# Kernel tuning notes

Measured on AMD Instinct MI355X. Metric: run time of the kernel, lower is better.

The kernel has to match this reference:

```python
import jax, jax.numpy as jnp
import numpy as np

N_FFT = 1024
HOP = 256
WIN = 1024


def _hann(win_length):
    # torch.hann_window (periodic): 0.5*(1 - cos(2*pi*n/N))
    n = jnp.arange(win_length, dtype=jnp.float32)
    return 0.5 - 0.5 * jnp.cos(2.0 * jnp.pi * n / win_length)


def setup_inputs() -> dict:
    key = jax.random.key(0)
    k1, k2 = jax.random.split(key)
    B, N, T = 16, N_FFT // 2 + 1, 2048
    spec_re = jax.random.normal(k1, (B, N, T), dtype=jnp.float32)
    spec_im = jax.random.normal(k2, (B, N, T), dtype=jnp.float32)
    mask = jnp.ones((B, T), dtype=jnp.float32)
    return {"spec_re": spec_re, "spec_im": spec_im, "mask": mask}


def reference(spec_re, spec_im, mask):
    B, N, T = spec_re.shape
    pad = (WIN - HOP) // 2
    window = _hann(WIN)

    spec = jax.lax.complex(spec_re, spec_im)
    # irfft over frequency axis, norm='backward' is jnp default -> [B, N_FFT, T]
    ifft = jnp.fft.irfft(spec, n=N_FFT, axis=1)
    # fuse window multiply + mask multiply
    frames = ifft * window[None, :, None] * mask[:, None, :]

    L = (T - 1) * HOP + WIN  # fold output size
    idx = jnp.arange(T)[None, :] * HOP + jnp.arange(WIN)[:, None]

    # fold(ifft): overlap-add of frames -> [B, L], then trim padding
    y = jnp.zeros((B, L), frames.dtype).at[:, idx].add(frames)[:, pad:L - pad]

    # window envelope (batch-independent): fold of window^2
    env = jnp.zeros((L,), frames.dtype).at[idx].add(
        jnp.broadcast_to((window * window)[:, None], (WIN, T))
    )[pad:L - pad]
    y = y / env

    # fold of ones*mask -> effective sample mask
    folded_mask = jnp.zeros((B, L), frames.dtype).at[:, idx].add(
        jnp.broadcast_to(mask[:, None, :], (B, WIN, T))
    )[:, pad:L - pad]
    effective_mask = (folded_mask > 0).astype(jnp.float32)
    return (y, effective_mask)
```

## Files before the change

### kernel.cpp

```cpp
#include <hip/hip_runtime.h>

#define THREADS 1024

#define BAR() do { asm volatile("s_waitcnt lgkmcnt(0)" ::: "memory"); \
                   __builtin_amdgcn_s_barrier();                      \
                   asm volatile("" ::: "memory"); } while (0)

__device__ __forceinline__ void dft8(float* vr, float* vi) {
    float t0r=vr[0]+vr[4], t0i=vi[0]+vi[4];
    float t1r=vr[0]-vr[4], t1i=vi[0]-vi[4];
    float t2r=vr[2]+vr[6], t2i=vi[2]+vi[6];
    float t3r=vr[2]-vr[6], t3i=vi[2]-vi[6];
    float t4r=vr[1]+vr[5], t4i=vi[1]+vi[5];
    float t5r=vr[1]-vr[5], t5i=vi[1]-vi[5];
    float t6r=vr[3]+vr[7], t6i=vi[3]+vi[7];
    float t7r=vr[3]-vr[7], t7i=vi[3]-vi[7];
    float e0r=t0r+t2r, e0i=t0i+t2i;
    float e1r=t1r-t3i, e1i=t1i+t3r;
    float e2r=t0r-t2r, e2i=t0i-t2i;
    float e3r=t1r+t3i, e3i=t1i-t3r;
    float o0r=t4r+t6r, o0i=t4i+t6i;
    float o1r=t5r-t7i, o1i=t5i+t7r;
    float o2r=t4r-t6r, o2i=t4i-t6i;
    float o3r=t5r+t7i, o3i=t5i-t7r;
    const float C = 0.70710678118654752f;
    float w1r = C*(o1r - o1i), w1i = C*(o1r + o1i);
    float w2r = -o2i,          w2i = o2r;
    float w3r = -C*(o3r + o3i), w3i = C*(o3r - o3i);
    vr[0]=e0r+o0r; vi[0]=e0i+o0i;
    vr[1]=e1r+w1r; vi[1]=e1i+w1i;
    vr[2]=e2r+w2r; vi[2]=e2i+w2i;
    vr[3]=e3r+w3r; vi[3]=e3i+w3i;
    vr[4]=e0r-o0r; vi[4]=e0i-o0i;
    vr[5]=e1r-w1r; vi[5]=e1i-w1i;
    vr[6]=e2r-w2r; vi[6]=e2i-w2i;
    vr[7]=e3r-w3r; vi[7]=e3i-w3i;
}

__device__ __forceinline__ void fft512(float* Re, float* Im, int l,
                                       const float2* s_twzb, const float2* s_tw64,
                                       const float2* s_tw512) {
    const int a_ = l >> 3, b_ = l & 7;
    float zr[8], zi[8];
    float cw = s_twzb[l].x, sw_ = s_twzb[l].y;
    const float C8 = 0.92387953251128675f, S8 = 0.38268343236508977f;
    #pragma unroll
    for (int k0 = 0; k0 < 8; ++k0) {
        int k = (k0<<6) + l;
        float xkr = Re[k],     xki = Im[k];
        float xmr = Re[512-k], xmi = Im[512-k];
        if (k == 0) { xki = 0.f; xmi = 0.f; }
        float Er = 0.5f*(xkr + xmr), Ei = 0.5f*(xki - xmi);
        float Dr = 0.5f*(xkr - xmr), Di = 0.5f*(xki + xmi);
        float Or = cw*Dr - sw_*Di,  Oi = sw_*Dr + cw*Di;
        zr[k0] = Er - Oi;
        zi[k0] = Ei + Or;
        float nc = cw*C8 - sw_*S8; sw_ = sw_*C8 + cw*S8; cw = nc;
    }
    dft8(zr, zi);
    #pragma unroll
    for (int q = 0; q < 8; ++q) {
        int idx = (q<<6) + l;
        Re[idx ^ (((idx>>6)&7)<<3)] = zr[q];
        Im[idx ^ (((idx>>6)&7)<<3)] = zi[q];
    }
    #pragma unroll
    for (int q = 0; q < 8; ++q) {
        int idx = (a_<<6) + (q<<3) + b_;
        int ph = idx ^ (((idx>>6)&7)<<3);
        zr[q] = Re[ph]; zi[q] = Im[ph];
    }
    {
        float c1 = s_tw64[a_].x, s1 = s_tw64[a_].y;
        float cr = c1, ci = s1;
        #pragma unroll
        for (int q = 1; q < 8; ++q) {
            float tr = zr[q]*cr - zi[q]*ci;
            zi[q] = zr[q]*ci + zi[q]*cr;
            zr[q] = tr;
            float nc = cr*c1 - ci*s1; ci = ci*c1 + cr*s1; cr = nc;
        }
    }
    dft8(zr, zi);
    #pragma unroll
    for (int q = 0; q < 8; ++q) {
        int idx = (b_<<6) + (q<<3) + a_;
        int ph = idx ^ (((idx>>6)&7)<<3);
        Re[ph] = zr[q]; Im[ph] = zi[q];
    }
    #pragma unroll
    for (int q = 0; q < 8; ++q) {
        int idx = (q<<6) + l;
        int ph = idx ^ (((idx>>6)&7)<<3);
        zr[q] = Re[ph]; zi[q] = Im[ph];
    }
    {
        float c1 = s_tw512[l].x, s1 = s_tw512[l].y;
        float cr = c1, ci = s1;
        #pragma unroll
        for (int q = 1; q < 8; ++q) {
            float tr = zr[q]*cr - zi[q]*ci;
            zi[q] = zr[q]*ci + zi[q]*cr;
            zr[q] = tr;
            float nc = cr*c1 - ci*s1; ci = ci*c1 + cr*s1; cr = nc;
        }
    }
    dft8(zr, zi);
    #pragma unroll
    for (int q = 0; q < 8; ++q) {
        Re[(q<<6) + l] = zr[q];
        Im[(q<<6) + l] = zi[q];
    }
}

template<bool USE_WS>
__global__ __launch_bounds__(1024, 8) void istft_main(const float* __restrict__ spec_re,
                                                      const float* __restrict__ spec_im,
                                                      const float* __restrict__ mask,
                                                      float* __restrict__ out,
                                                      float* __restrict__ wsL,
                                                      float* __restrict__ wsR)
{
    const int G   = blockIdx.x;
    const int b   = blockIdx.y;
    const int tid = threadIdx.x;

    __shared__ __attribute__((aligned(16))) float s_slot[16704];
    __shared__ __attribute__((aligned(16))) float s_wt[1024];
    __shared__ __attribute__((aligned(16))) float s_envr[256];
    __shared__ float  s_maskx[22];
    __shared__ float  s_ps[23];
    __shared__ float2 s_twzb[64];
    __shared__ float2 s_tw64[8];
    __shared__ float2 s_tw512[64];

    const size_t base = (size_t)b * 513 * 2048 + (size_t)(G * 16);
    const int c  = tid & 3;
    const int r0 = tid >> 2;
    float4 vr0, vi0, vr1, vi1, nyr, nyi;
    float4 mk;
    float mxv = 0.f;
    {
        size_t o0 = base + (size_t)(r0      ) * 2048 + (size_t)(c * 4);
        size_t o1 = base + (size_t)(r0 + 256) * 2048 + (size_t)(c * 4);
        vr0 = *(const float4*)(spec_re + o0);  vi0 = *(const float4*)(spec_im + o0);
        vr1 = *(const float4*)(spec_re + o1);  vi1 = *(const float4*)(spec_im + o1);
        if (tid < 4) {
            size_t o2 = base + (size_t)512 * 2048 + (size_t)(tid * 4);
            nyr = *(const float4*)(spec_re + o2);
            nyi = *(const float4*)(spec_im + o2);
        }
        mk = *(const float4*)(mask + b*2048 + G*16 + c*4);
        if (tid < 22) {
            int gf = G*16 - 3 + tid;
            mxv = (gf >= 0 && gf < 2048) ? mask[b*2048 + gf] : 0.f;
        }
    }

    {
        float w = 0.5f - 0.5f * __cosf(6.2831853071795864f * (float)tid * (1.0f/1024.0f));
        s_wt[tid] = w * (1.0f/512.0f);
    }
    if (tid < 256) {
        float e = 0.f;
        #pragma unroll
        for (int k = 0; k < 4; ++k) {
            float w = 0.5f - 0.5f * __cosf(6.2831853071795864f * (float)(tid + (k<<8)) * (1.0f/1024.0f));
            e += w * w;
        }
        s_envr[tid] = 1.0f / e;
    }
    if (tid < 64) {
        float s1, c1, s2, c2;
        __sincosf(3.1415926535897932f * (float)tid * (1.0f/512.0f), &s1, &c1);
        s_twzb[tid] = make_float2(c1, s1);
        __sincosf(6.2831853071795864f * (float)tid * (1.0f/512.0f), &s2, &c2);
        s_tw512[tid] = make_float2(c2, s2);
    }
    if (tid < 8) {
        float s3, c3;
        __sincosf(6.2831853071795864f * (float)tid * (1.0f/64.0f), &s3, &c3);
        s_tw64[tid] = make_float2(c3, s3);
    }
    if (tid < 22) s_maskx[tid] = mxv;

    {
        const float* mp = (const float*)&mk;
        #pragma unroll
        for (int f = 0; f < 4; ++f) {
            int fr = (c*4 + f) * 522;
            s_slot[       fr + r0      ] = ((const float*)&vr0)[f] * mp[f];
            s_slot[8352 + fr + r0      ] = ((const float*)&vi0)[f] * mp[f];
            s_slot[       fr + r0 + 256] = ((const float*)&vr1)[f] * mp[f];
            s_slot[8352 + fr + r0 + 256] = ((const float*)&vi1)[f] * mp[f];
        }
        if (tid < 4) {
            #pragma unroll
            for (int f = 0; f < 4; ++f) {
                int fr = (tid*4 + f) * 522;
                s_slot[       fr + 512] = ((const float*)&nyr)[f] * mp[f];
                s_slot[8352 + fr + 512] = ((const float*)&nyi)[f] * mp[f];
            }
        }
    }
    if (tid == 0) {
        float acc = 0.f;
        s_ps[0] = 0.f;
        #pragma unroll
        for (int i = 0; i < 22; ++i) { acc += s_maskx[i]; s_ps[i+1] = acc; }
    }
    BAR();

    __builtin_amdgcn_s_setprio(1);
    {
        const int wv = tid >> 6, l = tid & 63;
        fft512(&s_slot[wv*522], &s_slot[8352 + wv*522], l, s_twzb, s_tw64, s_tw512);
    }
    __builtin_amdgcn_s_setprio(0);
    BAR();

    const int P0 = G << 12;
    float* yout = out + (size_t)b * 524288;
    float* mout = out + 16ull*524288 + (size_t)b * 524288;

    {
        const int p0 = tid << 2;
        if (p0 >= 768) {
            const int F0 = (p0 >> 8) - 3;
            float4 acc = {0.f, 0.f, 0.f, 0.f};
            #pragma unroll
            for (int u = 0; u < 4; ++u) {
                int F = F0 + u;
                int j = p0 - (F << 8);
                float2 re = *(const float2*)&s_slot[       F*522 + (j >> 1)];
                float2 im = *(const float2*)&s_slot[8352 + F*522 + (j >> 1)];
                float4 w4 = *(const float4*)&s_wt[j];
                acc.x += re.x * w4.x;  acc.y += im.x * w4.y;
                acc.z += re.y * w4.z;  acc.w += im.y * w4.w;
            }
            float fm = s_ps[(p0 >> 8) + 4] - s_ps[F0 + 3];
            float m = (fm > 0.f) ? 1.0f : 0.0f;
            float4 er = *(const float4*)&s_envr[p0 & 255];
            int s = P0 + p0 - 384;
            float4 r;
            r.x = acc.x * er.x;  r.y = acc.y * er.y;
            r.z = acc.z * er.z;  r.w = acc.w * er.w;
            *(float4*)&yout[s] = r;
            float4 mm = {m, m, m, m};
            *(float4*)&mout[s] = mm;
        } else {
            const int thi = p0 >> 8;
            float4 acc = {0.f, 0.f, 0.f, 0.f};
            for (int F = 0; F <= thi; ++F) {
                int j = p0 - (F << 8);
                float2 re = *(const float2*)&s_slot[       F*522 + (j >> 1)];
                float2 im = *(const float2*)&s_slot[8352 + F*522 + (j >> 1)];
                float4 w4 = *(const float4*)&s_wt[j];
                acc.x += re.x * w4.x;  acc.y += im.x * w4.y;
                acc.z += re.y * w4.z;  acc.w += im.y * w4.w;
            }
            float fm = s_ps[thi + 4] - s_ps[((p0 - 768) >> 8) + 3];
            float m = (fm > 0.f) ? 1.0f : 0.0f;
            float4 mm = {m, m, m, m};
            if (G == 0) {
                if (p0 >= 384) {
                    float4 e = {0.f, 0.f, 0.f, 0.f};
                    for (int t = 0; t <= thi; ++t) {
                        float4 w4 = *(const float4*)&s_wt[p0 - (t << 8)];
                        e.x += w4.x * w4.x;  e.y += w4.y * w4.y;
                        e.z += w4.z * w4.z;  e.w += w4.w * w4.w;
                    }
                    const float S = 1.0f / 262144.0f;
                    float4 r;
                    r.x = acc.x * S / e.x;  r.y = acc.y * S / e.y;
                    r.z = acc.z * S / e.z;  r.w = acc.w * S / e.w;
                    *(float4*)&yout[p0 - 384] = r;
                    *(float4*)&mout[p0 - 384] = mm;
                }
            } else {
                int s = P0 + p0 - 384;
                if (USE_WS) {
                    *(float4*)&wsL[(size_t)((b << 7) + G) * 768 + p0] = acc;
                } else {
                    atomicAdd(&yout[s+0], acc.x);  atomicAdd(&yout[s+1], acc.y);
                    atomicAdd(&yout[s+2], acc.z);  atomicAdd(&yout[s+3], acc.w);
                }
                *(float4*)&mout[s] = mm;
            }
        }
    }
    if (tid < 192) {
        const int p0 = 4096 + (tid << 2);
        const int Flo = (p0 - 768) >> 8;
        float4 acc = {0.f, 0.f, 0.f, 0.f};
        for (int F = Flo; F < 16; ++F) {
            int j = p0 - (F << 8);
            float2 re = *(const float2*)&s_slot[       F*522 + (j >> 1)];
            float2 im = *(const float2*)&s_slot[8352 + F*522 + (j >> 1)];
            float4 w4 = *(const float4*)&s_wt[j];
            acc.x += re.x * w4.x;  acc.y += im.x * w4.y;
            acc.z += re.y * w4.z;  acc.w += im.y * w4.w;
        }
        float fm = s_ps[min(p0 >> 8, 18) + 4] - s_ps[Flo + 3];
        float m = (fm > 0.f) ? 1.0f : 0.0f;
        float4 mm = {m, m, m, m};
        if (G == 127) {
            if (p0 < 4480) {
                float4 e = {0.f, 0.f, 0.f, 0.f};
                for (int t = Flo; t < 16; ++t) {
                    float4 w4 = *(const float4*)&s_wt[p0 - (t << 8)];
                    e.x += w4.x * w4.x;  e.y += w4.y * w4.y;
                    e.z += w4.z * w4.z;  e.w += w4.w * w4.w;
                }
                const float S = 1.0f / 262144.0f;
                int s = P0 + p0 - 384;
                float4 r;
                r.x = acc.x * S / e.x;  r.y = acc.y * S / e.y;
                r.z = acc.z * S / e.z;  r.w = acc.w * S / e.w;
                *(float4*)&yout[s] = r;
                *(float4*)&mout[s] = mm;
            }
        } else {
            int s = P0 + p0 - 384;
            if (USE_WS) {
                *(float4*)&wsR[(size_t)((b << 7) + G) * 768 + (p0 - 4096)] = acc;
            } else {
                atomicAdd(&yout[s+0], acc.x);  atomicAdd(&yout[s+1], acc.y);
                atomicAdd(&yout[s+2], acc.z);  atomicAdd(&yout[s+3], acc.w);
            }
            *(float4*)&mout[s] = mm;
        }
    }
}

__global__ void istft_fixup_ws(const float* __restrict__ wsL, const float* __restrict__ wsR,
                               float* __restrict__ out) {
    int idx = blockIdx.x * 256 + threadIdx.x;
    if (idx >= 16*127*192) return;
    int q4 = (idx % 192) << 2;
    int t_ = idx / 192;
    int g  = (t_ % 127) + 1;
    int b  = t_ / 127;
    float4 aR = *(const float4*)&wsR[(size_t)((b << 7) + (g-1)) * 768 + q4];
    float4 aL = *(const float4*)&wsL[(size_t)((b << 7) + g) * 768 + q4];
    float4 r;
    #pragma unroll
    for (int cmp = 0; cmp < 4; ++cmp) {
        int j0 = (q4 + cmp) & 255;
        float e = 0.f;
        #pragma unroll
        for (int u = 0; u < 4; ++u) {
            float w = 0.5f - 0.5f * __cosf(6.2831853071795864f * (float)(j0 + (u<<8)) * (1.0f/1024.0f));
            e += w * w;
        }
        float a = ((const float*)&aR)[cmp] + ((const float*)&aL)[cmp];
        ((float*)&r)[cmp] = a / e;
    }
    *(float4*)&out[(size_t)b*524288 + (size_t)((g << 12) + q4 - 384)] = r;
}

__global__ void istft_zero(float* __restrict__ out) {
    int idx = blockIdx.x * 256 + threadIdx.x;
    if (idx >= 16*127*768) return;
    int q  = idx % 768;
    int t_ = idx / 768;
    int g  = (t_ % 127) + 1;
    int b  = t_ / 127;
    out[(size_t)b*524288 + (g << 12) + q - 384] = 0.f;
}

__global__ void istft_fixup_at(float* __restrict__ out) {
    int idx = blockIdx.x * 256 + threadIdx.x;
    if (idx >= 16*127*768) return;
    int q  = idx % 768;
    int t_ = idx / 768;
    int g  = (t_ % 127) + 1;
    int b  = t_ / 127;
    int j0 = q & 255;
    float e = 0.f;
    #pragma unroll
    for (int u = 0; u < 4; ++u) {
        float w = 0.5f - 0.5f * __cosf(6.2831853071795864f * (float)(j0 + (u<<8)) * (1.0f/1024.0f));
        e += w * w;
    }
    size_t o = (size_t)b*524288 + (size_t)((g << 12) + q - 384);
    out[o] = out[o] / e;
}

extern "C" void kernel_launch(void* const* d_in, const int* in_sizes, int n_in,
                              void* d_out, int out_size, void* d_ws, size_t ws_size,
                              hipStream_t stream) {
    (void)in_sizes; (void)n_in; (void)out_size;
    const float* spec_re = (const float*)d_in[0];
    const float* spec_im = (const float*)d_in[1];
    const float* mask    = (const float*)d_in[2];
    float* out = (float*)d_out;
    const size_t ws_need = 2ull * 16 * 128 * 768 * 4;
    if (ws_size >= ws_need && d_ws != nullptr) {
        float* wsL = (float*)d_ws;
        float* wsR = wsL + 16ull*128*768;
        istft_main<true><<<dim3(128, 16), 1024, 0, stream>>>(spec_re, spec_im, mask, out, wsL, wsR);
        const int nq = 16*127*192;
        istft_fixup_ws<<<(nq + 255)/256, 256, 0, stream>>>(wsL, wsR, out);
    } else {
        const int nstrip = 16*127*768;
        istft_zero<<<(nstrip + 255)/256, 256, 0, stream>>>(out);
        istft_main<false><<<dim3(128, 16), 1024, 0, stream>>>(spec_re, spec_im, mask, out, nullptr, nullptr);
        istft_fixup_at<<<(nstrip + 255)/256, 256, 0, stream>>>(out);
    }
}
```

Before: 77.81 us.

## Interleave complex FFT slots as float2 and use full twiddle tables

```diff
diff --git a/kernel.cpp b/kernel.cpp
--- a/kernel.cpp
+++ b/kernel.cpp
@@ -1,10 +1,13 @@
 #include <hip/hip_runtime.h>
 
 #define THREADS 1024
+#define CSTRIDE 514
 
 #define BAR() do { asm volatile("s_waitcnt lgkmcnt(0)" ::: "memory"); \
                    __builtin_amdgcn_s_barrier();                      \
                    asm volatile("" ::: "memory"); } while (0)
+
+__device__ __forceinline__ int swz(int i) { return i ^ (((i >> 6) & 7) << 3); }
 
 __device__ __forceinline__ void dft8(float* vr, float* vi) {
     float t0r=vr[0]+vr[4], t0i=vi[0]+vi[4];
@@ -37,21 +40,21 @@
     vr[7]=e3r-w3r; vi[7]=e3i-w3i;
 }
 
-__device__ __forceinline__ void fft512(float* Re, float* Im, int l,
-                                       const float2* s_twzb, const float2* s_tw64,
-                                       const float2* s_tw512) {
+__device__ __forceinline__ void fft512i(float2* S, int l,
+                                        const float2* twzb, const float2* tw64f,
+                                        const float2* tw512f) {
     const int a_ = l >> 3, b_ = l & 7;
     float zr[8], zi[8];
-    float cw = s_twzb[l].x, sw_ = s_twzb[l].y;
+    float cw = twzb[l].x, sw_ = twzb[l].y;
     const float C8 = 0.92387953251128675f, S8 = 0.38268343236508977f;
     #pragma unroll
     for (int k0 = 0; k0 < 8; ++k0) {
         int k = (k0<<6) + l;
-        float xkr = Re[k],     xki = Im[k];
-        float xmr = Re[512-k], xmi = Im[512-k];
-        if (k == 0) { xki = 0.f; xmi = 0.f; }
-        float Er = 0.5f*(xkr + xmr), Ei = 0.5f*(xki - xmi);
-        float Dr = 0.5f*(xkr - xmr), Di = 0.5f*(xki + xmi);
+        float2 xk = S[swz(k)];
+        float2 xm = S[swz(512-k)];
+        if (k == 0) { xk.y = 0.f; xm.y = 0.f; }
+        float Er = 0.5f*(xk.x + xm.x), Ei = 0.5f*(xk.y - xm.y);
+        float Dr = 0.5f*(xk.x - xm.x), Di = 0.5f*(xk.y + xm.y);
         float Or = cw*Dr - sw_*Di,  Oi = sw_*Dr + cw*Di;
         zr[k0] = Er - Oi;
         zi[k0] = Ei + Or;
@@ -59,58 +62,40 @@
     }
     dft8(zr, zi);
     #pragma unroll
+    for (int q = 0; q < 8; ++q)
+        S[swz((q<<6) + l)] = make_float2(zr[q], zi[q]);
+    #pragma unroll
     for (int q = 0; q < 8; ++q) {
-        int idx = (q<<6) + l;
-        Re[idx ^ (((idx>>6)&7)<<3)] = zr[q];
-        Im[idx ^ (((idx>>6)&7)<<3)] = zi[q];
-    }
+        float2 t = S[swz((a_<<6) + (q<<3) + b_)];
+        zr[q] = t.x; zi[q] = t.y;
+    }
+    #pragma unroll
+    for (int q = 1; q < 8; ++q) {
+        float2 w = tw64f[(a_*q) & 63];
+        float tr = zr[q]*w.x - zi[q]*w.y;
+        zi[q] = zr[q]*w.y + zi[q]*w.x;
+        zr[q] = tr;
+    }
+    dft8(zr, zi);
+    #pragma unroll
+    for (int q = 0; q < 8; ++q)
+        S[swz((b_<<6) + (q<<3) + a_)] = make_float2(zr[q], zi[q]);
     #pragma unroll
     for (int q = 0; q < 8; ++q) {
-        int idx = (a_<<6) + (q<<3) + b_;
-        int ph = idx ^ (((idx>>6)&7)<<3);
-        zr[q] = Re[ph]; zi[q] = Im[ph];
-    }
-    {
-        float c1 = s_tw64[a_].x, s1 = s_tw64[a_].y;
-        float cr = c1, ci = s1;
-        #pragma unroll
-        for (int q = 1; q < 8; ++q) {
-            float tr = zr[q]*cr - zi[q]*ci;
-            zi[q] = zr[q]*ci + zi[q]*cr;
-            zr[q] = tr;
-            float nc = cr*c1 - ci*s1; ci = ci*c1 + cr*s1; cr = nc;
-        }
+        float2 t = S[swz((q<<6) + l)];
+        zr[q] = t.x; zi[q] = t.y;
+    }
+    #pragma unroll
+    for (int q = 1; q < 8; ++q) {
+        float2 w = tw512f[(l*q) & 511];
+        float tr = zr[q]*w.x - zi[q]*w.y;
+        zi[q] = zr[q]*w.y + zi[q]*w.x;
+        zr[q] = tr;
     }
     dft8(zr, zi);
     #pragma unroll
-    for (int q = 0; q < 8; ++q) {
-        int idx = (b_<<6) + (q<<3) + a_;
-        int ph = idx ^ (((idx>>6)&7)<<3);
-        Re[ph] = zr[q]; Im[ph] = zi[q];
-    }
-    #pragma unroll
-    for (int q = 0; q < 8; ++q) {
-        int idx = (q<<6) + l;
-        int ph = idx ^ (((idx>>6)&7)<<3);
-        zr[q] = Re[ph]; zi[q] = Im[ph];
-    }
-    {
-        float c1 = s_tw512[l].x, s1 = s_tw512[l].y;
-        float cr = c1, ci = s1;
-        #pragma unroll
-        for (int q = 1; q < 8; ++q) {
-            float tr = zr[q]*cr - zi[q]*ci;
-            zi[q] = zr[q]*ci + zi[q]*cr;
-            zr[q] = tr;
-            float nc = cr*c1 - ci*s1; ci = ci*c1 + cr*s1; cr = nc;
-        }
-    }
-    dft8(zr, zi);
-    #pragma unroll
-    for (int q = 0; q < 8; ++q) {
-        Re[(q<<6) + l] = zr[q];
-        Im[(q<<6) + l] = zi[q];
-    }
+    for (int q = 0; q < 8; ++q)
+        S[swz((q<<6) + l)] = make_float2(zr[q], zi[q]);
 }
 
 template<bool USE_WS>
@@ -125,14 +110,14 @@
     const int b   = blockIdx.y;
     const int tid = threadIdx.x;
 
-    __shared__ __attribute__((aligned(16))) float s_slot[16704];
-    __shared__ __attribute__((aligned(16))) float s_wt[1024];
-    __shared__ __attribute__((aligned(16))) float s_envr[256];
+    __shared__ __attribute__((aligned(16))) float2 s_slot[16*CSTRIDE];
+    __shared__ __attribute__((aligned(16))) float  s_wt[1024];
+    __shared__ __attribute__((aligned(16))) float  s_envr[256];
     __shared__ float  s_maskx[22];
     __shared__ float  s_ps[23];
     __shared__ float2 s_twzb[64];
-    __shared__ float2 s_tw64[8];
-    __shared__ float2 s_tw512[64];
+    __shared__ float2 s_tw64f[64];
+    __shared__ float2 s_tw512f[512];
 
     const size_t base = (size_t)b * 513 * 2048 + (size_t)(G * 16);
     const int c  = tid & 3;
@@ -161,6 +146,11 @@
         float w = 0.5f - 0.5f * __cosf(6.2831853071795864f * (float)tid * (1.0f/1024.0f));
         s_wt[tid] = w * (1.0f/512.0f);
     }
+    if (tid < 512) {
+        float s2, c2;
+        __sincosf(6.2831853071795864f * (float)tid * (1.0f/512.0f), &s2, &c2);
+        s_tw512f[tid] = make_float2(c2, s2);
+    }
     if (tid < 256) {
         float e = 0.f;
         #pragma unroll
@@ -171,16 +161,11 @@
         s_envr[tid] = 1.0f / e;
     }
     if (tid < 64) {
-        float s1, c1, s2, c2;
+        float s1, c1, s3, c3;
         __sincosf(3.1415926535897932f * (float)tid * (1.0f/512.0f), &s1, &c1);
         s_twzb[tid] = make_float2(c1, s1);
-        __sincosf(6.2831853071795864f * (float)tid * (1.0f/512.0f), &s2, &c2);
-        s_tw512[tid] = make_float2(c2, s2);
-    }
-    if (tid < 8) {
-        float s3, c3;
         __sincosf(6.2831853071795864f * (float)tid * (1.0f/64.0f), &s3, &c3);
-        s_tw64[tid] = make_float2(c3, s3);
+        s_tw64f[tid] = make_float2(c3, s3);
     }
     if (tid < 22) s_maskx[tid] = mxv;
 
@@ -188,19 +173,18 @@
         const float* mp = (const float*)&mk;
         #pragma unroll
         for (int f = 0; f < 4; ++f) {
-            int fr = (c*4 + f) * 522;
-            s_slot[       fr + r0      ] = ((const float*)&vr0)[f] * mp[f];
-            s_slot[8352 + fr + r0      ] = ((const float*)&vi0)[f] * mp[f];
-            s_slot[       fr + r0 + 256] = ((const float*)&vr1)[f] * mp[f];
-            s_slot[8352 + fr + r0 + 256] = ((const float*)&vi1)[f] * mp[f];
+            float2* SF = &s_slot[(c*4 + f) * CSTRIDE];
+            SF[swz(r0      )] = make_float2(((const float*)&vr0)[f] * mp[f],
+                                            ((const float*)&vi0)[f] * mp[f]);
+            SF[swz(r0 + 256)] = make_float2(((const float*)&vr1)[f] * mp[f],
+                                            ((const float*)&vi1)[f] * mp[f]);
         }
         if (tid < 4) {
             #pragma unroll
-            for (int f = 0; f < 4; ++f) {
-                int fr = (tid*4 + f) * 522;
-                s_slot[       fr + 512] = ((const float*)&nyr)[f] * mp[f];
-                s_slot[8352 + fr + 512] = ((const float*)&nyi)[f] * mp[f];
-            }
+            for (int f = 0; f < 4; ++f)
+                s_slot[(tid*4 + f) * CSTRIDE + 512] =
+                    make_float2(((const float*)&nyr)[f] * mp[f],
+                                ((const float*)&nyi)[f] * mp[f]);
         }
     }
     if (tid == 0) {
@@ -214,7 +198,7 @@
     __builtin_amdgcn_s_setprio(1);
     {
         const int wv = tid >> 6, l = tid & 63;
-        fft512(&s_slot[wv*522], &s_slot[8352 + wv*522], l, s_twzb, s_tw64, s_tw512);
+        fft512i(&s_slot[wv*CSTRIDE], l, s_twzb, s_tw64f, s_tw512f);
     }
     __builtin_amdgcn_s_setprio(0);
     BAR();
@@ -231,12 +215,11 @@
             #pragma unroll
             for (int u = 0; u < 4; ++u) {
                 int F = F0 + u;
-                int j = p0 - (F << 8);
-                float2 re = *(const float2*)&s_slot[       F*522 + (j >> 1)];
-                float2 im = *(const float2*)&s_slot[8352 + F*522 + (j >> 1)];
-                float4 w4 = *(const float4*)&s_wt[j];
-                acc.x += re.x * w4.x;  acc.y += im.x * w4.y;
-                acc.z += re.y * w4.z;  acc.w += im.y * w4.w;
+                int e = (p0 >> 1) - (F << 7);
+                float4 v  = *(const float4*)&s_slot[F*CSTRIDE + swz(e)];
+                float4 w4 = *(const float4*)&s_wt[p0 - (F << 8)];
+                acc.x += v.x * w4.x;  acc.y += v.y * w4.y;
+                acc.z += v.z * w4.z;  acc.w += v.w * w4.w;
             }
             float fm = s_ps[(p0 >> 8) + 4] - s_ps[F0 + 3];
             float m = (fm > 0.f) ? 1.0f : 0.0f;
@@ -252,12 +235,11 @@
             const int thi = p0 >> 8;
             float4 acc = {0.f, 0.f, 0.f, 0.f};
             for (int F = 0; F <= thi; ++F) {
-                int j = p0 - (F << 8);
-                float2 re = *(const float2*)&s_slot[       F*522 + (j >> 1)];
-                float2 im = *(const float2*)&s_slot[8352 + F*522 + (j >> 1)];
-                float4 w4 = *(const float4*)&s_wt[j];
-                acc.x += re.x * w4.x;  acc.y += im.x * w4.y;
-                acc.z += re.y * w4.z;  acc.w += im.y * w4.w;
+                int e = (p0 >> 1) - (F << 7);
+                float4 v  = *(const float4*)&s_slot[F*CSTRIDE + swz(e)];
+                float4 w4 = *(const float4*)&s_wt[p0 - (F << 8)];
+                acc.x += v.x * w4.x;  acc.y += v.y * w4.y;
+                acc.z += v.z * w4.z;  acc.w += v.w * w4.w;
             }
             float fm = s_ps[thi + 4] - s_ps[((p0 - 768) >> 8) + 3];
             float m = (fm > 0.f) ? 1.0f : 0.0f;
@@ -294,12 +276,11 @@
         const int Flo = (p0 - 768) >> 8;
         float4 acc = {0.f, 0.f, 0.f, 0.f};
         for (int F = Flo; F < 16; ++F) {
-            int j = p0 - (F << 8);
-            float2 re = *(const float2*)&s_slot[       F*522 + (j >> 1)];
-            float2 im = *(const float2*)&s_slot[8352 + F*522 + (j >> 1)];
-            float4 w4 = *(const float4*)&s_wt[j];
-            acc.x += re.x * w4.x;  acc.y += im.x * w4.y;
-            acc.z += re.y * w4.z;  acc.w += im.y * w4.w;
+            int e = (p0 >> 1) - (F << 7);
+            float4 v  = *(const float4*)&s_slot[F*CSTRIDE + swz(e)];
+            float4 w4 = *(const float4*)&s_wt[p0 - (F << 8)];
+            acc.x += v.x * w4.x;  acc.y += v.y * w4.y;
+            acc.z += v.z * w4.z;  acc.w += v.w * w4.w;
         }
         float fm = s_ps[min(p0 >> 8, 18) + 4] - s_ps[Flo + 3];
         float m = (fm > 0.f) ? 1.0f : 0.0f;
```

New measurement: 78.81 us. No clear change (+1.3%).

## Process four frame groups per block with carried overlap and prefetched loads

Applied to the files above, without the earlier changes.

```diff
diff --git a/kernel.cpp b/kernel.cpp
--- a/kernel.cpp
+++ b/kernel.cpp
@@ -1,6 +1,4 @@
 #include <hip/hip_runtime.h>
-
-#define THREADS 1024
 
 #define BAR() do { asm volatile("s_waitcnt lgkmcnt(0)" ::: "memory"); \
                    __builtin_amdgcn_s_barrier();                      \
@@ -121,7 +119,7 @@
                                                       float* __restrict__ wsL,
                                                       float* __restrict__ wsR)
 {
-    const int G   = blockIdx.x;
+    const int g2  = blockIdx.x;
     const int b   = blockIdx.y;
     const int tid = threadIdx.x;
 
@@ -134,29 +132,31 @@
     __shared__ float2 s_tw64[8];
     __shared__ float2 s_tw512[64];
 
-    const size_t base = (size_t)b * 513 * 2048 + (size_t)(G * 16);
     const int c  = tid & 3;
     const int r0 = tid >> 2;
-    float4 vr0, vi0, vr1, vi1, nyr, nyi;
-    float4 mk;
-    float mxv = 0.f;
-    {
-        size_t o0 = base + (size_t)(r0      ) * 2048 + (size_t)(c * 4);
-        size_t o1 = base + (size_t)(r0 + 256) * 2048 + (size_t)(c * 4);
-        vr0 = *(const float4*)(spec_re + o0);  vi0 = *(const float4*)(spec_im + o0);
-        vr1 = *(const float4*)(spec_re + o1);  vi1 = *(const float4*)(spec_im + o1);
-        if (tid < 4) {
-            size_t o2 = base + (size_t)512 * 2048 + (size_t)(tid * 4);
-            nyr = *(const float4*)(spec_re + o2);
-            nyi = *(const float4*)(spec_im + o2);
-        }
-        mk = *(const float4*)(mask + b*2048 + G*16 + c*4);
-        if (tid < 22) {
-            int gf = G*16 - 3 + tid;
-            mxv = (gf >= 0 && gf < 2048) ? mask[b*2048 + gf] : 0.f;
-        }
-    }
-
+    float4 vr0, vi0, vr1, vi1, nyr, nyi, mk;
+    float  mxv = 0.f;
+
+#define ISSUE_LOADS(GG) do {                                                     \
+        size_t base_ = (size_t)b * 513 * 2048 + (size_t)((GG) * 16);             \
+        size_t o0_ = base_ + (size_t)(r0      ) * 2048 + (size_t)(c * 4);        \
+        size_t o1_ = base_ + (size_t)(r0 + 256) * 2048 + (size_t)(c * 4);        \
+        vr0 = *(const float4*)(spec_re + o0_);  vi0 = *(const float4*)(spec_im + o0_); \
+        vr1 = *(const float4*)(spec_re + o1_);  vi1 = *(const float4*)(spec_im + o1_); \
+        if (tid < 4) {                                                           \
+            size_t o2_ = base_ + (size_t)512 * 2048 + (size_t)(tid * 4);         \
+            nyr = *(const float4*)(spec_re + o2_);                               \
+            nyi = *(const float4*)(spec_im + o2_);                               \
+        }                                                                        \
+        mk = *(const float4*)(mask + b*2048 + (GG)*16 + c*4);                    \
+        if (tid < 22) {                                                          \
+            int gf_ = (GG)*16 - 3 + tid;                                         \
+            mxv = (gf_ >= 0 && gf_ < 2048) ? mask[b*2048 + gf_] : 0.f;           \
+        }                                                                        \
+    } while (0)
+
+    const int G0 = g2 << 2;
+    ISSUE_LOADS(G0);
     {
         float w = 0.5f - 0.5f * __cosf(6.2831853071795864f * (float)tid * (1.0f/1024.0f));
         s_wt[tid] = w * (1.0f/512.0f);
@@ -182,55 +182,134 @@
         __sincosf(6.2831853071795864f * (float)tid * (1.0f/64.0f), &s3, &c3);
         s_tw64[tid] = make_float2(c3, s3);
     }
-    if (tid < 22) s_maskx[tid] = mxv;
-
-    {
-        const float* mp = (const float*)&mk;
-        #pragma unroll
-        for (int f = 0; f < 4; ++f) {
-            int fr = (c*4 + f) * 522;
-            s_slot[       fr + r0      ] = ((const float*)&vr0)[f] * mp[f];
-            s_slot[8352 + fr + r0      ] = ((const float*)&vi0)[f] * mp[f];
-            s_slot[       fr + r0 + 256] = ((const float*)&vr1)[f] * mp[f];
-            s_slot[8352 + fr + r0 + 256] = ((const float*)&vi1)[f] * mp[f];
-        }
-        if (tid < 4) {
+
+    float* yout = out + (size_t)b * 524288;
+    float* mout = out + 16ull*524288 + (size_t)b * 524288;
+    float4 carry = {0.f, 0.f, 0.f, 0.f};
+
+    for (int t = 0; t < 4; ++t) {
+        const int G  = G0 + t;
+        const int P0 = G << 12;
+
+        if (tid < 22) s_maskx[tid] = mxv;
+        {
+            const float* mp = (const float*)&mk;
             #pragma unroll
             for (int f = 0; f < 4; ++f) {
-                int fr = (tid*4 + f) * 522;
-                s_slot[       fr + 512] = ((const float*)&nyr)[f] * mp[f];
-                s_slot[8352 + fr + 512] = ((const float*)&nyi)[f] * mp[f];
+                int fr = (c*4 + f) * 522;
+                s_slot[       fr + r0      ] = ((const float*)&vr0)[f] * mp[f];
+                s_slot[8352 + fr + r0      ] = ((const float*)&vi0)[f] * mp[f];
+                s_slot[       fr + r0 + 256] = ((const float*)&vr1)[f] * mp[f];
+                s_slot[8352 + fr + r0 + 256] = ((const float*)&vi1)[f] * mp[f];
             }
-        }
-    }
-    if (tid == 0) {
-        float acc = 0.f;
-        s_ps[0] = 0.f;
-        #pragma unroll
-        for (int i = 0; i < 22; ++i) { acc += s_maskx[i]; s_ps[i+1] = acc; }
-    }
-    BAR();
-
-    __builtin_amdgcn_s_setprio(1);
-    {
-        const int wv = tid >> 6, l = tid & 63;
-        fft512(&s_slot[wv*522], &s_slot[8352 + wv*522], l, s_twzb, s_tw64, s_tw512);
-    }
-    __builtin_amdgcn_s_setprio(0);
-    BAR();
-
-    const int P0 = G << 12;
-    float* yout = out + (size_t)b * 524288;
-    float* mout = out + 16ull*524288 + (size_t)b * 524288;
-
-    {
-        const int p0 = tid << 2;
-        if (p0 >= 768) {
-            const int F0 = (p0 >> 8) - 3;
+            if (tid < 4) {
+                #pragma unroll
+                for (int f = 0; f < 4; ++f) {
+                    int fr = (tid*4 + f) * 522;
+                    s_slot[       fr + 512] = ((const float*)&nyr)[f] * mp[f];
+                    s_slot[8352 + fr + 512] = ((const float*)&nyi)[f] * mp[f];
+                }
+            }
+        }
+        if (tid == 0) {
+            float acc = 0.f;
+            s_ps[0] = 0.f;
+            #pragma unroll
+            for (int i = 0; i < 22; ++i) { acc += s_maskx[i]; s_ps[i+1] = acc; }
+        }
+        BAR();
+
+        __builtin_amdgcn_s_setprio(1);
+        {
+            const int wv = tid >> 6, l = tid & 63;
+            fft512(&s_slot[wv*522], &s_slot[8352 + wv*522], l, s_twzb, s_tw64, s_tw512);
+        }
+        __builtin_amdgcn_s_setprio(0);
+        BAR();
+
+        if (t < 3) ISSUE_LOADS(G + 1);
+
+        {
+            const int p0 = tid << 2;
+            if (p0 >= 768) {
+                const int F0 = (p0 >> 8) - 3;
+                float4 acc = {0.f, 0.f, 0.f, 0.f};
+                #pragma unroll
+                for (int u = 0; u < 4; ++u) {
+                    int F = F0 + u;
+                    int j = p0 - (F << 8);
+                    float2 re = *(const float2*)&s_slot[       F*522 + (j >> 1)];
+                    float2 im = *(const float2*)&s_slot[8352 + F*522 + (j >> 1)];
+                    float4 w4 = *(const float4*)&s_wt[j];
+                    acc.x += re.x * w4.x;  acc.y += im.x * w4.y;
+                    acc.z += re.y * w4.z;  acc.w += im.y * w4.w;
+                }
+                float fm = s_ps[(p0 >> 8) + 4] - s_ps[F0 + 3];
+                float m = (fm > 0.f) ? 1.0f : 0.0f;
+                float4 er = *(const float4*)&s_envr[p0 & 255];
+                int s = P0 + p0 - 384;
+                float4 r;
+                r.x = acc.x * er.x;  r.y = acc.y * er.y;
+                r.z = acc.z * er.z;  r.w = acc.w * er.w;
+                *(float4*)&yout[s] = r;
+                float4 mm = {m, m, m, m};
+                *(float4*)&mout[s] = mm;
+            } else {
+                const int thi = p0 >> 8;
+                float4 acc = {0.f, 0.f, 0.f, 0.f};
+                for (int F = 0; F <= thi; ++F) {
+                    int j = p0 - (F << 8);
+                    float2 re = *(const float2*)&s_slot[       F*522 + (j >> 1)];
+                    float2 im = *(const float2*)&s_slot[8352 + F*522 + (j >> 1)];
+                    float4 w4 = *(const float4*)&s_wt[j];
+                    acc.x += re.x * w4.x;  acc.y += im.x * w4.y;
+                    acc.z += re.y * w4.z;  acc.w += im.y * w4.w;
+                }
+                float fm = s_ps[thi + 4] - s_ps[((p0 - 768) >> 8) + 3];
+                float m = (fm > 0.f) ? 1.0f : 0.0f;
+                float4 mm = {m, m, m, m};
+                if (t > 0) {
+                    acc.x += carry.x;  acc.y += carry.y;
+                    acc.z += carry.z;  acc.w += carry.w;
+                    float4 er = *(const float4*)&s_envr[p0 & 255];
+                    int s = P0 + p0 - 384;
+                    float4 r;
+                    r.x = acc.x * er.x;  r.y = acc.y * er.y;
+                    r.z = acc.z * er.z;  r.w = acc.w * er.w;
+                    *(float4*)&yout[s] = r;
+                    *(float4*)&mout[s] = mm;
+                } else if (G == 0) {
+                    if (p0 >= 384) {
+                        float4 e = {0.f, 0.f, 0.f, 0.f};
+                        for (int tt = 0; tt <= thi; ++tt) {
+                            float4 w4 = *(const float4*)&s_wt[p0 - (tt << 8)];
+                            e.x += w4.x * w4.x;  e.y += w4.y * w4.y;
+                            e.z += w4.z * w4.z;  e.w += w4.w * w4.w;
+                        }
+                        const float S = 1.0f / 262144.0f;
+                        float4 r;
+                        r.x = acc.x * S / e.x;  r.y = acc.y * S / e.y;
+                        r.z = acc.z * S / e.z;  r.w = acc.w * S / e.w;
+                        *(float4*)&yout[p0 - 384] = r;
+                        *(float4*)&mout[p0 - 384] = mm;
+                    }
+                } else {
+                    int s = P0 + p0 - 384;
+                    if (USE_WS) {
+                        *(float4*)&wsL[(size_t)((b << 7) + G) * 768 + p0] = acc;
+                    } else {
+                        atomicAdd(&yout[s+0], acc.x);  atomicAdd(&yout[s+1], acc.y);
+                        atomicAdd(&yout[s+2], acc.z);  atomicAdd(&yout[s+3], acc.w);
+                    }
+                    *(float4*)&mout[s] = mm;
+                }
+            }
+        }
+        if (tid < 192) {
+            const int p0 = 4096 + (tid << 2);
+            const int Flo = (p0 - 768) >> 8;
             float4 acc = {0.f, 0.f, 0.f, 0.f};
-            #pragma unroll
-            for (int u = 0; u < 4; ++u) {
-                int F = F0 + u;
+            for (int F = Flo; F < 16; ++F) {
                 int j = p0 - (F << 8);
                 float2 re = *(const float2*)&s_slot[       F*522 + (j >> 1)];
                 float2 im = *(const float2*)&s_slot[8352 + F*522 + (j >> 1)];
@@ -238,49 +317,34 @@
                 acc.x += re.x * w4.x;  acc.y += im.x * w4.y;
                 acc.z += re.y * w4.z;  acc.w += im.y * w4.w;
             }
-            float fm = s_ps[(p0 >> 8) + 4] - s_ps[F0 + 3];
-            float m = (fm > 0.f) ? 1.0f : 0.0f;
-            float4 er = *(const float4*)&s_envr[p0 & 255];
-            int s = P0 + p0 - 384;
-            float4 r;
-            r.x = acc.x * er.x;  r.y = acc.y * er.y;
-            r.z = acc.z * er.z;  r.w = acc.w * er.w;
-            *(float4*)&yout[s] = r;
-            float4 mm = {m, m, m, m};
-            *(float4*)&mout[s] = mm;
-        } else {
-            const int thi = p0 >> 8;
-            float4 acc = {0.f, 0.f, 0.f, 0.f};
-            for (int F = 0; F <= thi; ++F) {
-                int j = p0 - (F << 8);
-                float2 re = *(const float2*)&s_slot[       F*522 + (j >> 1)];
-                float2 im = *(const float2*)&s_slot[8352 + F*522 + (j >> 1)];
-                float4 w4 = *(const float4*)&s_wt[j];
-                acc.x += re.x * w4.x;  acc.y += im.x * w4.y;
-                acc.z += re.y * w4.z;  acc.w += im.y * w4.w;
-            }
-            float fm = s_ps[thi + 4] - s_ps[((p0 - 768) >> 8) + 3];
-            float m = (fm > 0.f) ? 1.0f : 0.0f;
-            float4 mm = {m, m, m, m};
-            if (G == 0) {
-                if (p0 >= 384) {
+            if (t < 3) {
+                carry = acc;
+            } else if (G == 127) {
+                if (p0 < 4480) {
+                    float fm = s_ps[min(p0 >> 8, 18) + 4] - s_ps[Flo + 3];
+                    float m = (fm > 0.f) ? 1.0f : 0.0f;
+                    float4 mm = {m, m, m, m};
                     float4 e = {0.f, 0.f, 0.f, 0.f};
-                    for (int t = 0; t <= thi; ++t) {
-                        float4 w4 = *(const float4*)&s_wt[p0 - (t << 8)];
+                    for (int tt = Flo; tt < 16; ++tt) {
+                        float4 w4 = *(const float4*)&s_wt[p0 - (tt << 8)];
                         e.x += w4.x * w4.x;  e.y += w4.y * w4.y;
                         e.z += w4.z * w4.z;  e.w += w4.w * w4.w;
                     }
                     const float S = 1.0f / 262144.0f;
+                    int s = P0 + p0 - 384;
                     float4 r;
                     r.x = acc.x * S / e.x;  r.y = acc.y * S / e.y;
                     r.z = acc.z * S / e.z;  r.w = acc.w * S / e.w;
-                    *(float4*)&yout[p0 - 384] = r;
-                    *(float4*)&mout[p0 - 384] = mm;
+                    *(float4*)&yout[s] = r;
+                    *(float4*)&mout[s] = mm;
                 }
             } else {
+                float fm = s_ps[min(p0 >> 8, 18) + 4] - s_ps[Flo + 3];
+                float m = (fm > 0.f) ? 1.0f : 0.0f;
+                float4 mm = {m, m, m, m};
                 int s = P0 + p0 - 384;
                 if (USE_WS) {
-                    *(float4*)&wsL[(size_t)((b << 7) + G) * 768 + p0] = acc;
+                    *(float4*)&wsR[(size_t)((b << 7) + G) * 768 + (p0 - 4096)] = acc;
                 } else {
                     atomicAdd(&yout[s+0], acc.x);  atomicAdd(&yout[s+1], acc.y);
                     atomicAdd(&yout[s+2], acc.z);  atomicAdd(&yout[s+3], acc.w);
@@ -288,59 +352,19 @@
                 *(float4*)&mout[s] = mm;
             }
         }
-    }
-    if (tid < 192) {
-        const int p0 = 4096 + (tid << 2);
-        const int Flo = (p0 - 768) >> 8;
-        float4 acc = {0.f, 0.f, 0.f, 0.f};
-        for (int F = Flo; F < 16; ++F) {
-            int j = p0 - (F << 8);
-            float2 re = *(const float2*)&s_slot[       F*522 + (j >> 1)];
-            float2 im = *(const float2*)&s_slot[8352 + F*522 + (j >> 1)];
-            float4 w4 = *(const float4*)&s_wt[j];
-            acc.x += re.x * w4.x;  acc.y += im.x * w4.y;
-            acc.z += re.y * w4.z;  acc.w += im.y * w4.w;
-        }
-        float fm = s_ps[min(p0 >> 8, 18) + 4] - s_ps[Flo + 3];
-        float m = (fm > 0.f) ? 1.0f : 0.0f;
-        float4 mm = {m, m, m, m};
-        if (G == 127) {
-            if (p0 < 4480) {
-                float4 e = {0.f, 0.f, 0.f, 0.f};
-                for (int t = Flo; t < 16; ++t) {
-                    float4 w4 = *(const float4*)&s_wt[p0 - (t << 8)];
-                    e.x += w4.x * w4.x;  e.y += w4.y * w4.y;
-                    e.z += w4.z * w4.z;  e.w += w4.w * w4.w;
-                }
-                const float S = 1.0f / 262144.0f;
-                int s = P0 + p0 - 384;
-                float4 r;
-                r.x = acc.x * S / e.x;  r.y = acc.y * S / e.y;
-                r.z = acc.z * S / e.z;  r.w = acc.w * S / e.w;
-                *(float4*)&yout[s] = r;
-                *(float4*)&mout[s] = mm;
-            }
-        } else {
-            int s = P0 + p0 - 384;
-            if (USE_WS) {
-                *(float4*)&wsR[(size_t)((b << 7) + G) * 768 + (p0 - 4096)] = acc;
-            } else {
-                atomicAdd(&yout[s+0], acc.x);  atomicAdd(&yout[s+1], acc.y);
-                atomicAdd(&yout[s+2], acc.z);  atomicAdd(&yout[s+3], acc.w);
-            }
-            *(float4*)&mout[s] = mm;
-        }
-    }
+        if (t < 3) BAR();
+    }
+#undef ISSUE_LOADS
 }
 
 __global__ void istft_fixup_ws(const float* __restrict__ wsL, const float* __restrict__ wsR,
                                float* __restrict__ out) {
     int idx = blockIdx.x * 256 + threadIdx.x;
-    if (idx >= 16*127*192) return;
+    if (idx >= 16*31*192) return;
     int q4 = (idx % 192) << 2;
     int t_ = idx / 192;
-    int g  = (t_ % 127) + 1;
-    int b  = t_ / 127;
+    int g  = ((t_ % 31) + 1) << 2;
+    int b  = t_ / 31;
     float4 aR = *(const float4*)&wsR[(size_t)((b << 7) + (g-1)) * 768 + q4];
     float4 aL = *(const float4*)&wsL[(size_t)((b << 7) + g) * 768 + q4];
     float4 r;
@@ -361,21 +385,21 @@
 
 __global__ void istft_zero(float* __restrict__ out) {
     int idx = blockIdx.x * 256 + threadIdx.x;
-    if (idx >= 16*127*768) return;
+    if (idx >= 16*31*768) return;
     int q  = idx % 768;
     int t_ = idx / 768;
-    int g  = (t_ % 127) + 1;
-    int b  = t_ / 127;
+    int g  = ((t_ % 31) + 1) << 2;
+    int b  = t_ / 31;
     out[(size_t)b*524288 + (g << 12) + q - 384] = 0.f;
 }
 
 __global__ void istft_fixup_at(float* __restrict__ out) {
     int idx = blockIdx.x * 256 + threadIdx.x;
-    if (idx >= 16*127*768) return;
+    if (idx >= 16*31*768) return;
     int q  = idx % 768;
     int t_ = idx / 768;
-    int g  = (t_ % 127) + 1;
-    int b  = t_ / 127;
+    int g  = ((t_ % 31) + 1) << 2;
+    int b  = t_ / 31;
     int j0 = q & 255;
     float e = 0.f;
     #pragma unroll
@@ -399,13 +423,13 @@
     if (ws_size >= ws_need && d_ws != nullptr) {
         float* wsL = (float*)d_ws;
         float* wsR = wsL + 16ull*128*768;
-        istft_main<true><<<dim3(128, 16), 1024, 0, stream>>>(spec_re, spec_im, mask, out, wsL, wsR);
-        const int nq = 16*127*192;
+        istft_main<true><<<dim3(32, 16), 1024, 0, stream>>>(spec_re, spec_im, mask, out, wsL, wsR);
+        const int nq = 16*31*192;
         istft_fixup_ws<<<(nq + 255)/256, 256, 0, stream>>>(wsL, wsR, out);
     } else {
-        const int nstrip = 16*127*768;
+        const int nstrip = 16*31*768;
         istft_zero<<<(nstrip + 255)/256, 256, 0, stream>>>(out);
-        istft_main<false><<<dim3(128, 16), 1024, 0, stream>>>(spec_re, spec_im, mask, out, nullptr, nullptr);
+        istft_main<false><<<dim3(32, 16), 1024, 0, stream>>>(spec_re, spec_im, mask, out, nullptr, nullptr);
         istft_fixup_at<<<(nstrip + 255)/256, 256, 0, stream>>>(out);
     }
 }
```

After: 157.0 us. 2.02x slower.
